# Kernel optimization log

Hardware: AMD Instinct MI355X
Metric: run time of the kernel (lower is better)

## Reference

```python
import jax, jax.numpy as jnp
import numpy as np
from jax import lax


def conv2d(x, w, b=None, pad=1):
    y = lax.conv_general_dilated(x, w, (1, 1), [(pad, pad), (pad, pad)],
                                 dimension_numbers=('NCHW', 'OIHW', 'NCHW'))
    return y if b is None else y + b[None, :, None, None]


def conv3d(x, w, b=None, pad=(0, 0, 0), dil=(1, 1, 1), groups=1):
    y = lax.conv_general_dilated(x, w, (1, 1, 1), [(p, p) for p in pad],
                                 rhs_dilation=dil,
                                 dimension_numbers=('NCDHW', 'OIDHW', 'NCDHW'),
                                 feature_group_count=groups)
    return y if b is None else y + b[None, :, None, None, None]


def base_grid(H, W, dtype):
    # normalized grid, channel 0 = x in [-1,1], channel 1 = y in [-1,1]
    gxn = 2.0 * jnp.arange(W, dtype=dtype) / max(W - 1, 1) - 1.0
    gyn = 2.0 * jnp.arange(H, dtype=dtype) / max(H - 1, 1) - 1.0
    return jnp.stack([jnp.broadcast_to(gxn[None, :], (H, W)),
                      jnp.broadcast_to(gyn[:, None], (H, W))], 0)


def grid_sample(img, grid):
    # img (N,C,H,W), grid (N,H,W,2) in [-1,1] (x,y); bilinear, zeros padding, align_corners=False
    N, C, H, W = img.shape
    gx = ((grid[..., 0] + 1.0) * W - 1.0) * 0.5
    gy = ((grid[..., 1] + 1.0) * H - 1.0) * 0.5
    x0 = jnp.floor(gx)
    y0 = jnp.floor(gy)
    wx = gx - x0
    wy = gy - y0

    def one(im, x0b, y0b, wxb, wyb):
        x0i = x0b.astype(jnp.int32)
        y0i = y0b.astype(jnp.int32)

        def samp(xi, yi):
            valid = (xi >= 0) & (xi < W) & (yi >= 0) & (yi < H)
            v = im[:, jnp.clip(yi, 0, H - 1), jnp.clip(xi, 0, W - 1)]
            return v * valid[None].astype(im.dtype)

        v00 = samp(x0i, y0i)
        v01 = samp(x0i + 1, y0i)
        v10 = samp(x0i, y0i + 1)
        v11 = samp(x0i + 1, y0i + 1)
        return (v00 * (1 - wxb) * (1 - wyb) + v01 * wxb * (1 - wyb)
                + v10 * (1 - wxb) * wyb + v11 * wxb * wyb)

    return jax.vmap(one)(img, x0, y0, wx, wy)


def ms_def_corr(x, y, off):
    # deformable correlation: per scale, warp y by that scale's offset and take
    # the channel-mean dot product with x -> (BT, S, H, W)
    BT, C, H, W = x.shape
    base = base_grid(H, W, x.dtype)
    sc = jnp.array([W - 1, H - 1], x.dtype)[None, :, None, None]
    S = off.shape[1] // 2
    corrs = []
    for i in range(S):
        vg = base[None] + off[:, 2 * i:2 * i + 2] / sc
        w = grid_sample(y, vg.transpose(0, 2, 3, 1))
        corrs.append(jnp.mean(x * w, axis=1))
    return jnp.stack(corrs, 1)


def corr_filter(corr, w1, w2):
    avg = jnp.mean(corr, 1, keepdims=True)
    mx = jnp.max(corr, 1, keepdims=True)
    var = jnp.var(corr, axis=1, keepdims=True, ddof=1)  # torch.var unbiased
    attn = jax.nn.sigmoid(conv2d(jnp.concatenate([avg, mx], 1), w1) + conv2d(var, w2))
    return corr * attn


def setup_inputs() -> dict:
    key = jax.random.key(0)
    ks = jax.random.split(key, 16)
    B, C, T, H, W = 2, 64, 16, 64, 64
    S = 3
    r = C // 16

    def n(k, shape, s=0.02):
        return jax.random.normal(k, shape, jnp.float32) * s

    return {
        'x': jax.random.normal(ks[0], (B, C, T, H, W), jnp.float32),
        'ofs_l_w1': n(ks[1], (C, 2 * C, 3, 3)), 'ofs_l_b1': jnp.zeros((C,), jnp.float32),
        'ofs_l_w2': n(ks[2], (2 * S, C, 3, 3)), 'ofs_l_b2': jnp.zeros((2 * S,), jnp.float32),
        'ofs_r_w1': n(ks[3], (C, 2 * C, 3, 3)), 'ofs_r_b1': jnp.zeros((C,), jnp.float32),
        'ofs_r_w2': n(ks[4], (2 * S, C, 3, 3)), 'ofs_r_b2': jnp.zeros((2 * S,), jnp.float32),
        'cf_w1': n(ks[5], (1, 2, 3, 3), 0.1), 'cf_w2': n(ks[6], (1, 1, 3, 3), 0.1),
        'down_w': n(ks[7], (r, C, 1, 1, 1), 0.1),
        'sa1_w': n(ks[8], (r, 1, 9, 3, 3), 0.1), 'sa1_b': jnp.zeros((r,), jnp.float32),
        'sa2_w': n(ks[9], (r, 1, 9, 3, 3), 0.1), 'sa2_b': jnp.zeros((r,), jnp.float32),
        'sa3_w': n(ks[10], (r, 1, 9, 3, 3), 0.1), 'sa3_b': jnp.zeros((r,), jnp.float32),
        'agg_w': jnp.ones((3,), jnp.float32) / 3,
        'back_w': n(ks[11], (C, r, 1, 1, 1), 0.1),
        'fusion_w': jnp.ones((2,), jnp.float32) / 2,
    }


def reference(x, ofs_l_w1, ofs_l_b1, ofs_l_w2, ofs_l_b2,
              ofs_r_w1, ofs_r_b1, ofs_r_w2, ofs_r_b2,
              cf_w1, cf_w2, down_w,
              sa1_w, sa1_b, sa2_w, sa2_b, sa3_w, sa3_b,
              agg_w, back_w, fusion_w):
    B, C, T, H, W = x.shape
    r = down_w.shape[0]

    # long-term branch: 1x1x1 down conv -> 3 dilated depthwise 3D convs -> 1x1x1 up conv
    x_agg = conv3d(x, down_w)
    agg = (conv3d(x_agg, sa1_w, sa1_b, (4, 1, 1), (1, 1, 1), r) * agg_w[0]
           + conv3d(x_agg, sa2_w, sa2_b, (4, 2, 2), (1, 2, 2), r) * agg_w[1]
           + conv3d(x_agg, sa3_w, sa3_b, (4, 3, 3), (1, 3, 3), r) * agg_w[2])
    long_term = jax.nn.sigmoid(conv3d(agg, back_w)) - 0.5

    # temporal shifts
    left = jnp.concatenate([x[:, :, 1:], x[:, :, -1:]], 2)
    right = jnp.concatenate([x[:, :, :1], x[:, :, :-1]], 2)
    xf = x.transpose(0, 2, 1, 3, 4).reshape(B * T, C, H, W)
    lf = left.transpose(0, 2, 1, 3, 4).reshape(B * T, C, H, W)
    rf = right.transpose(0, 2, 1, 3, 4).reshape(B * T, C, H, W)

    off_lm = conv2d(jax.nn.relu(conv2d(jnp.concatenate([xf, lf], 1), ofs_l_w1, ofs_l_b1)),
                    ofs_l_w2, ofs_l_b2)
    off_rm = conv2d(jax.nn.relu(conv2d(jnp.concatenate([xf, rf], 1), ofs_r_w1, ofs_r_b1)),
                    ofs_r_w2, ofs_r_b2)

    corr_lm = ms_def_corr(xf, lf, off_lm)
    corr_rm = ms_def_corr(xf, rf, off_rm)
    fcl = corr_filter(corr_lm, cf_w1, cf_w2)
    fcr = corr_filter(corr_rm, cf_w1, cf_w2)

    base = base_grid(H, W, x.dtype)
    sc = jnp.array([W - 1, H - 1], x.dtype)[None, :, None, None]
    vg_lm = base[None] + off_lm[:, :2] / sc
    vg_rm = base[None] + off_rm[:, :2] / sc
    warped_lm = grid_sample(lf, vg_lm.transpose(0, 2, 3, 1))
    warped_rm = grid_sample(rf, vg_rm.transpose(0, 2, 3, 1))

    attn_lm = jnp.mean(fcl, 1, keepdims=True)
    attn_rm = jnp.mean(fcr, 1, keepdims=True)
    feat_lm = warped_lm * (jax.nn.sigmoid(attn_lm) - 0.5)
    feat_rm = warped_rm * (jax.nn.sigmoid(attn_rm) - 0.5)

    short = fusion_w[0] * feat_lm + fusion_w[1] * feat_rm
    short = short.reshape(B, T, C, H, W).transpose(0, 2, 1, 3, 4)
    return short * long_term
```

## Files before the change

kernel.cpp:

```cpp
#include <hip/hip_runtime.h>
#include <hip/hip_bf16.h>
#include <math.h>


typedef __attribute__((ext_vector_type(8))) short short8v;
typedef __attribute__((ext_vector_type(4))) float f32x4;

__device__ __forceinline__ float sigmoidf_(float v) {
    return 1.0f / (1.0f + expf(-v));
}

__device__ __forceinline__ float bf2f(short s) {
    union { unsigned u; float f; } z;
    z.u = ((unsigned)(unsigned short)s) << 16;
    return z.f;
}

__device__ __forceinline__ void gll16(const __hip_bfloat16* g, __hip_bfloat16* l) {
    __builtin_amdgcn_global_load_lds((const __attribute__((address_space(1))) unsigned int*)(const void*)g,
                                     (__attribute__((address_space(3))) unsigned int*)(void*)l,
                                     16, 0, 0);
}

struct Samp { int o0, o1, o2, o3; float w0, w1, w2, w3; };

__device__ __forceinline__ Samp make_samp(float ox, float oy, int w, int h) {
    float bx = (2.0f * (float)w) / 63.0f - 1.0f;
    float by = (2.0f * (float)h) / 63.0f - 1.0f;
    float vx = bx + ox / 63.0f;
    float vy = by + oy / 63.0f;
    float gx = ((vx + 1.0f) * 64.0f - 1.0f) * 0.5f;
    float gy = ((vy + 1.0f) * 64.0f - 1.0f) * 0.5f;
    float fx = floorf(gx), fy = floorf(gy);
    float wx = gx - fx, wy = gy - fy;
    int x0 = (int)fx, y0 = (int)fy;
    int x1 = x0 + 1, y1 = y0 + 1;
    bool vx0 = (x0 >= 0) && (x0 < 64), vx1 = (x1 >= 0) && (x1 < 64);
    bool vy0 = (y0 >= 0) && (y0 < 64), vy1 = (y1 >= 0) && (y1 < 64);
    int cx0 = min(max(x0, 0), 63), cx1 = min(max(x1, 0), 63);
    int cy0 = min(max(y0, 0), 63), cy1 = min(max(y1, 0), 63);
    Samp s;
    s.o0 = cy0 * 4224 + (cx0 + 1) * 64; s.w0 = (1.0f - wx) * (1.0f - wy) * ((vx0 && vy0) ? 1.0f : 0.0f);
    s.o1 = cy0 * 4224 + (cx1 + 1) * 64; s.w1 = wx * (1.0f - wy) * ((vx1 && vy0) ? 1.0f : 0.0f);
    s.o2 = cy1 * 4224 + (cx0 + 1) * 64; s.w2 = (1.0f - wx) * wy * ((vx0 && vy1) ? 1.0f : 0.0f);
    s.o3 = cy1 * 4224 + (cx1 + 1) * 64; s.w3 = wx * wy * ((vx1 && vy1) ? 1.0f : 0.0f);
    return s;
}

__global__ __launch_bounds__(256) void k_prep_x(const float* __restrict__ x,
                                                const float* __restrict__ dw,
                                                __hip_bfloat16* __restrict__ xT,
                                                float* __restrict__ xa)
{
    int bid = blockIdx.x;
    int h = bid & 63;
    int n = bid >> 6;
    int b = n >> 4, t = n & 15;
    __shared__ float s[64][65];
    int tid = threadIdx.x;
    for (int idx = tid; idx < 4096; idx += 256) {
        int c = idx >> 6, w = idx & 63;
        s[c][w] = x[(((size_t)b * 64 + c) * 16 + t) * 4096 + h * 64 + w];
    }
    __syncthreads();
    __hip_bfloat16* op = xT + ((size_t)n * 64 + h) * 4224;
    for (int idx = tid; idx < 4224; idx += 256) {
        int wp = idx >> 6, c = idx & 63;
        float v = (wp == 0 || wp == 65) ? 0.f : s[c][wp - 1];
        op[idx] = __float2bfloat16(v);
    }
    int w = tid & 63, g = tid >> 6;
    float acc = 0.f;
    const float* dwg = dw + g * 64;
    #pragma unroll 8
    for (int c = 0; c < 64; c++) acc = fmaf(s[c][w], dwg[c], acc);
    xa[((size_t)(b * 4 + g) * 16 + t) * 4096 + h * 64 + w] = acc;
}

__global__ __launch_bounds__(256) void k_prep_w(const float* __restrict__ wl1,
                                                const float* __restrict__ wr1,
                                                const float* __restrict__ wl2,
                                                const float* __restrict__ wr2,
                                                __hip_bfloat16* __restrict__ Wmisc,
                                                __hip_bfloat16* __restrict__ hidden)
{
    int idx = blockIdx.x * 256 + threadIdx.x;
    if (idx < 147456) {
        int side = (idx >= 73728) ? 1 : 0;
        int i = idx - side * 73728;
        int ci = i & 127;
        int co = (i >> 7) & 63;
        int tap = i >> 13;
        const float* w = side ? wr1 : wl1;
        float v = w[((size_t)co * 128 + ci) * 9 + tap];
        int pos = side * 73728 + tap * 8192 + co * 128 + (ci ^ ((co & 15) << 3));
        Wmisc[pos] = __float2bfloat16(v);
    } else if (idx < 151680) {
        Wmisc[idx] = __float2bfloat16(0.f);
    } else if (idx < 170112) {
        int i2 = idx - 151680;
        int side = i2 / 9216;
        int j = i2 - side * 9216;
        int tap = j >> 10;
        int rem = j & 1023;
        int co = rem >> 6;
        int ci = rem & 63;
        const float* w = side ? wr2 : wl2;
        float v = (co < 6) ? w[((size_t)co * 64 + ci) * 9 + tap] : 0.f;
        Wmisc[idx] = __float2bfloat16(v);
    } else if (idx < 432256) {
        int i3 = idx - 170112;
        int co = i3 & 63;
        int sel = (i3 >> 6) & 1;
        int rr = (i3 >> 7) & 63;
        int nn = i3 >> 13;
        hidden[((size_t)(nn * 64 + rr) * 66 + (sel ? 65 : 0)) * 64 + co] = __float2bfloat16(0.f);
    }
}

__global__ __launch_bounds__(512, 4) void k_conv1_mfma(const __hip_bfloat16* __restrict__ xT,
                                                       const __hip_bfloat16* __restrict__ Wb,
                                                       const __hip_bfloat16* __restrict__ zrow,
                                                       const float* __restrict__ b1,
                                                       __hip_bfloat16* __restrict__ hidden,
                                                       int dir)
{
    __shared__ __hip_bfloat16 sB[24576];

    int bid = blockIdx.x;
    int rq = bid & 15;
    int n = bid >> 4;
    int b = n >> 4, t = n & 15;
    int t2 = (dir > 0) ? min(t + 1, 15) : max(t - 1, 0);
    int n2 = b * 16 + t2;

    int tid = threadIdx.x;
    int wv = tid >> 6;
    int lane = tid & 63;
    int r = rq * 4 + (wv & 3);
    int m0 = (wv >> 2) * 32;
    int lr = lane & 15;
    int q = lane >> 4;
    int lk = q << 3;

    const __hip_bfloat16* fA0 = xT + (size_t)n * 270336;
    const __hip_bfloat16* fA1 = xT + (size_t)n2 * 270336;

    f32x4 acc[2][4];
    #pragma unroll
    for (int ni = 0; ni < 4; ni++) {
        float bb = b1[ni * 16 + lr];
        acc[0][ni] = (f32x4){bb, bb, bb, bb};
        acc[1][ni] = (f32x4){bb, bb, bb, bb};
    }

    int kx[2][2];
    #pragma unroll
    for (int khalf = 0; khalf < 2; khalf++)
        #pragma unroll
        for (int ks = 0; ks < 2; ks++)
            kx[khalf][ks] = ((khalf << 7) + (ks << 6) + (q << 4)) ^ (lr << 4);

    const char* sbc = (const char*)&sB[0];

    #pragma unroll
    for (int g = 0; g < 3; g++) {
        __syncthreads();
        {
            const __hip_bfloat16* wsrc = Wb + (size_t)g * 24576 + wv * 3072 + lane * 8;
            #pragma unroll
            for (int j = 0; j < 6; j++)
                gll16(wsrc + j * 512, &sB[wv * 3072 + j * 512]);
        }
        __syncthreads();

        int rr = r + g - 1;
        bool ok = (rr >= 0) && (rr < 64);
        const __hip_bfloat16* r0 = ok ? (fA0 + rr * 4224) : zrow;
        const __hip_bfloat16* r1 = ok ? (fA1 + rr * 4224) : zrow;

        #pragma unroll
        for (int tl = 0; tl < 3; tl++) {
            int abase = (m0 + lr + tl) * 64 + lk;
            #pragma unroll
            for (int khalf = 0; khalf < 2; khalf++) {
                const __hip_bfloat16* ar = khalf ? r1 : r0;
                short8v a00 = *(const short8v*)(ar + abase);
                short8v a01 = *(const short8v*)(ar + abase + 32);
                short8v a10 = *(const short8v*)(ar + abase + 1024);
                short8v a11 = *(const short8v*)(ar + abase + 1056);
                #pragma unroll
                for (int ni = 0; ni < 4; ni++) {
                    int rowb = tl * 16384 + ni * 4096 + lr * 256;
                    short8v b0  = *(const short8v*)(sbc + (rowb + kx[khalf][0]));
                    short8v b1v = *(const short8v*)(sbc + (rowb + kx[khalf][1]));
                    acc[0][ni] = __builtin_amdgcn_mfma_f32_16x16x32_bf16(a00, b0, acc[0][ni], 0, 0, 0);
                    acc[1][ni] = __builtin_amdgcn_mfma_f32_16x16x32_bf16(a10, b0, acc[1][ni], 0, 0, 0);
                    acc[0][ni] = __builtin_amdgcn_mfma_f32_16x16x32_bf16(a01, b1v, acc[0][ni], 0, 0, 0);
                    acc[1][ni] = __builtin_amdgcn_mfma_f32_16x16x32_bf16(a11, b1v, acc[1][ni], 0, 0, 0);
                }
            }
        }
    }

    int pxq = q << 2;
    __hip_bfloat16* hb = hidden + (size_t)(n * 64 + r) * 66 * 64;
    #pragma unroll
    for (int mi = 0; mi < 2; mi++) {
        #pragma unroll
        for (int ni = 0; ni < 4; ni++) {
            int co = ni * 16 + lr;
            #pragma unroll
            for (int j = 0; j < 4; j++) {
                int px = m0 + mi * 16 + pxq + j;
                float v = acc[mi][ni][j];
                v = v < 0.f ? 0.f : v;
                hb[(size_t)(px + 1) * 64 + co] = __float2bfloat16(v);
            }
        }
    }
}

__global__ __launch_bounds__(256) void k_conv2_mfma(const __hip_bfloat16* __restrict__ hidden,
                                                    const __hip_bfloat16* __restrict__ W2b,
                                                    const __hip_bfloat16* __restrict__ zrow,
                                                    const float* __restrict__ b2,
                                                    float* __restrict__ off)
{
    int bid = blockIdx.x;
    int rq = bid & 15;
    int n = bid >> 4;
    int tid = threadIdx.x;
    int wv = tid >> 6;
    int lane = tid & 63;
    int r = rq * 4 + wv;
    int lr = lane & 15;
    int lk = (lane >> 4) << 3;

    const __hip_bfloat16* hbase = hidden + (size_t)n * 270336;

    float bb = (lr < 6) ? b2[lr] : 0.f;
    f32x4 acc[4];
    #pragma unroll
    for (int mi = 0; mi < 4; mi++) acc[mi] = (f32x4){bb, bb, bb, bb};

    #pragma unroll
    for (int tap = 0; tap < 9; tap++) {
        const int kh = tap / 3, kw = tap - (tap / 3) * 3;
        int rr = r + kh - 1;
        bool ok = (rr >= 0) && (rr < 64);
        const __hip_bfloat16* hr = ok ? (hbase + (size_t)rr * 4224) : zrow;
        const __hip_bfloat16* bw = W2b + ((size_t)tap * 16 + lr) * 64 + lk;
        short8v b0 = *(const short8v*)(bw);
        short8v b1v = *(const short8v*)(bw + 32);
        #pragma unroll
        for (int mi = 0; mi < 4; mi++) {
            int abase = (mi * 16 + lr + kw) * 64 + lk;
            short8v a0 = *(const short8v*)(hr + abase);
            short8v a1 = *(const short8v*)(hr + abase + 32);
            acc[mi] = __builtin_amdgcn_mfma_f32_16x16x32_bf16(a0, b0, acc[mi], 0, 0, 0);
            acc[mi] = __builtin_amdgcn_mfma_f32_16x16x32_bf16(a1, b1v, acc[mi], 0, 0, 0);
        }
    }
    if (lr < 6) {
        int pxq = (lane >> 4) << 2;
        #pragma unroll
        for (int mi = 0; mi < 4; mi++) {
            #pragma unroll
            for (int j = 0; j < 4; j++) {
                int px = mi * 16 + pxq + j;
                off[((size_t)n * 6 + lr) * 4096 + r * 64 + px] = acc[mi][j];
            }
        }
    }
}

__global__ __launch_bounds__(256) void k_agg(const float* __restrict__ xa,
                                             const float* __restrict__ w1, const float* __restrict__ b1,
                                             const float* __restrict__ w2, const float* __restrict__ b2,
                                             const float* __restrict__ w3, const float* __restrict__ b3,
                                             const float* __restrict__ aw,
                                             float* __restrict__ agg)
{
    int gid = blockIdx.x * 256 + threadIdx.x;
    int hw = gid & 4095;
    int rest = gid >> 12;
    int t = rest & 15;
    int g = (rest >> 4) & 3;
    int b = rest >> 6;
    int h = hw >> 6, w = hw & 63;
    const float* base = xa + ((size_t)(b * 4 + g) * 16) * 4096;
    const float* ws0 = w1 + g * 81;
    const float* ws1 = w2 + g * 81;
    const float* ws2 = w3 + g * 81;
    float acc0 = b1[g], acc1 = b2[g], acc2 = b3[g];
    for (int kd = 0; kd < 9; kd++) {
        int d = t + kd - 4;
        if (d < 0 || d > 15) continue;
        const float* fr = base + (size_t)d * 4096;
        #pragma unroll
        for (int kh = 0; kh < 3; kh++) {
            #pragma unroll
            for (int kw = 0; kw < 3; kw++) {
                int widx = kd * 9 + kh * 3 + kw;
                {
                    int yy = h + (kh - 1), xx = w + (kw - 1);
                    if (yy >= 0 && yy < 64 && xx >= 0 && xx < 64)
                        acc0 = fmaf(fr[yy * 64 + xx], ws0[widx], acc0);
                }
                {
                    int yy = h + (kh - 1) * 2, xx = w + (kw - 1) * 2;
                    if (yy >= 0 && yy < 64 && xx >= 0 && xx < 64)
                        acc1 = fmaf(fr[yy * 64 + xx], ws1[widx], acc1);
                }
                {
                    int yy = h + (kh - 1) * 3, xx = w + (kw - 1) * 3;
                    if (yy >= 0 && yy < 64 && xx >= 0 && xx < 64)
                        acc2 = fmaf(fr[yy * 64 + xx], ws2[widx], acc2);
                }
            }
        }
    }
    agg[gid] = acc0 * aw[0] + acc1 * aw[1] + acc2 * aw[2];
}

__global__ __launch_bounds__(256) void k_corr2(const __hip_bfloat16* __restrict__ xT,
                                               const float* __restrict__ off_l,
                                               const float* __restrict__ off_r,
                                               float* __restrict__ stats_l,
                                               float* __restrict__ stats_r)
{
    int tid = threadIdx.x;
    int wv = tid >> 6;
    int lane = tid & 63;
    int pl = lane & 31;
    int ch = lane >> 5;
    int pidx = blockIdx.x * 128 + wv * 32 + pl;
    int half = pidx >> 17;
    int gid = pidx & 131071;
    const float* off = half ? off_r : off_l;
    float* stats = half ? stats_r : stats_l;

    int hw = gid & 4095;
    int n = gid >> 12;
    int b = n >> 4, t = n & 15;
    int t2 = half ? max(t - 1, 0) : min(t + 1, 15);
    int n2 = b * 16 + t2;
    int h = hw >> 6, w = hw & 63;
    int cc0 = ch * 32;

    const __hip_bfloat16* xf = xT + (size_t)n * 270336 + h * 4224 + (w + 1) * 64 + cc0;
    const __hip_bfloat16* yf = xT + (size_t)n2 * 270336 + cc0;

    Samp sp[3];
    #pragma unroll
    for (int s = 0; s < 3; s++) {
        float ox = off[((size_t)n * 6 + 2 * s) * 4096 + hw];
        float oy = off[((size_t)n * 6 + 2 * s + 1) * 4096 + hw];
        sp[s] = make_samp(ox, oy, w, h);
    }

    short8v xv[4];
    #pragma unroll
    for (int i = 0; i < 4; i++) xv[i] = *(const short8v*)(xf + 8 * i);

    float ac[3][4];
    #pragma unroll
    for (int s = 0; s < 3; s++)
        #pragma unroll
        for (int qq = 0; qq < 4; qq++) ac[s][qq] = 0.f;

    #pragma unroll
    for (int s = 0; s < 3; s++) {
        #pragma unroll
        for (int pr = 0; pr < 2; pr++) {
            int oa = pr ? sp[s].o2 : sp[s].o0;
            int ob = pr ? sp[s].o3 : sp[s].o1;
            short8v va[4], vb[4];
            #pragma unroll
            for (int i = 0; i < 4; i++) {
                va[i] = *(const short8v*)(yf + oa + 8 * i);
                vb[i] = *(const short8v*)(yf + ob + 8 * i);
            }
            #pragma unroll
            for (int i = 0; i < 4; i++) {
                #pragma unroll
                for (int e = 0; e < 8; e++) {
                    float xe = bf2f(xv[i][e]);
                    ac[s][pr * 2]     = fmaf(xe, bf2f(va[i][e]), ac[s][pr * 2]);
                    ac[s][pr * 2 + 1] = fmaf(xe, bf2f(vb[i][e]), ac[s][pr * 2 + 1]);
                }
            }
        }
    }

    #pragma unroll
    for (int s = 0; s < 3; s++)
        #pragma unroll
        for (int qq = 0; qq < 4; qq++)
            ac[s][qq] += __shfl_xor(ac[s][qq], 32, 64);

    if (ch == 0) {
        float c[3];
        #pragma unroll
        for (int s = 0; s < 3; s++)
            c[s] = (ac[s][0] * sp[s].w0 + ac[s][1] * sp[s].w1 + ac[s][2] * sp[s].w2 + ac[s][3] * sp[s].w3) * (1.0f / 64.0f);
        float avg = (c[0] + c[1] + c[2]) * (1.0f / 3.0f);
        float mx = fmaxf(c[0], fmaxf(c[1], c[2]));
        float d0 = c[0] - avg, d1 = c[1] - avg, d2 = c[2] - avg;
        float var = (d0 * d0 + d1 * d1 + d2 * d2) * 0.5f;
        stats[(size_t)n * 4096 + hw] = avg;
        stats[131072 + (size_t)n * 4096 + hw] = mx;
        stats[262144 + (size_t)n * 4096 + hw] = var;
    }
}

__device__ __forceinline__ float attn_val(const float* __restrict__ stats, int n, int hw,
                                          const float* __restrict__ cfw1,
                                          const float* __restrict__ cfw2)
{
    int h = hw >> 6, w = hw & 63;
    const float* avg = stats + (size_t)n * 4096;
    const float* mx  = stats + 131072 + (size_t)n * 4096;
    const float* var = stats + 262144 + (size_t)n * 4096;
    float s = 0.f;
    #pragma unroll
    for (int k = 0; k < 9; k++) {
        int kh = k / 3 - 1, kw = k - (k / 3) * 3 - 1;
        int yy = h + kh, xx = w + kw;
        if (yy >= 0 && yy < 64 && xx >= 0 && xx < 64) {
            int p = yy * 64 + xx;
            s += avg[p] * cfw1[k] + mx[p] * cfw1[9 + k] + var[p] * cfw2[k];
        }
    }
    float attn = sigmoidf_(s);
    return sigmoidf_(avg[hw] * attn) - 0.5f;
}

__global__ __launch_bounds__(256) void k_final(const __hip_bfloat16* __restrict__ xT,
                                               const float* __restrict__ off_l,
                                               const float* __restrict__ off_r,
                                               const float* __restrict__ stats_l,
                                               const float* __restrict__ stats_r,
                                               const float* __restrict__ cfw1,
                                               const float* __restrict__ cfw2,
                                               const float* __restrict__ agg,
                                               const float* __restrict__ backw,
                                               const float* __restrict__ fusw,
                                               float* __restrict__ out)
{
    int gid0 = blockIdx.x * 256 + threadIdx.x;
    int hw = gid0 & 4095;
    int ch = (gid0 >> 12) & 1;
    int n = gid0 >> 13;
    int b = n >> 4, t = n & 15;
    int tl = min(t + 1, 15), tr = max(t - 1, 0);
    int nl = b * 16 + tl, nr = b * 16 + tr;
    int h = hw >> 6, w = hw & 63;
    int cc0 = ch * 32;

    float oxl = off_l[((size_t)n * 6 + 0) * 4096 + hw];
    float oyl = off_l[((size_t)n * 6 + 1) * 4096 + hw];
    float oxr = off_r[((size_t)n * 6 + 0) * 4096 + hw];
    float oyr = off_r[((size_t)n * 6 + 1) * 4096 + hw];
    Samp sl = make_samp(oxl, oyl, w, h);
    Samp sr = make_samp(oxr, oyr, w, h);

    const __hip_bfloat16* lf = xT + (size_t)nl * 270336 + cc0;
    const __hip_bfloat16* rf = xT + (size_t)nr * 270336 + cc0;

    short8v lv[4][4], rv[4][4];
    #pragma unroll
    for (int i = 0; i < 4; i++) {
        lv[0][i] = *(const short8v*)(lf + sl.o0 + 8 * i);
        lv[1][i] = *(const short8v*)(lf + sl.o1 + 8 * i);
        lv[2][i] = *(const short8v*)(lf + sl.o2 + 8 * i);
        lv[3][i] = *(const short8v*)(lf + sl.o3 + 8 * i);
        rv[0][i] = *(const short8v*)(rf + sr.o0 + 8 * i);
        rv[1][i] = *(const short8v*)(rf + sr.o1 + 8 * i);
        rv[2][i] = *(const short8v*)(rf + sr.o2 + 8 * i);
        rv[3][i] = *(const short8v*)(rf + sr.o3 + 8 * i);
    }

    float Al = attn_val(stats_l, n, hw, cfw1, cfw2) * fusw[0];
    float Ar = attn_val(stats_r, n, hw, cfw1, cfw2) * fusw[1];

    float ag0 = agg[((size_t)(b * 4 + 0) * 16 + t) * 4096 + hw];
    float ag1 = agg[((size_t)(b * 4 + 1) * 16 + t) * 4096 + hw];
    float ag2 = agg[((size_t)(b * 4 + 2) * 16 + t) * 4096 + hw];
    float ag3 = agg[((size_t)(b * 4 + 3) * 16 + t) * 4096 + hw];

    #pragma unroll
    for (int i = 0; i < 4; i++) {
        #pragma unroll
        for (int e = 0; e < 8; e++) {
            int c = cc0 + i * 8 + e;
            float wl = sl.w0 * bf2f(lv[0][i][e]) + sl.w1 * bf2f(lv[1][i][e])
                     + sl.w2 * bf2f(lv[2][i][e]) + sl.w3 * bf2f(lv[3][i][e]);
            float wr = sr.w0 * bf2f(rv[0][i][e]) + sr.w1 * bf2f(rv[1][i][e])
                     + sr.w2 * bf2f(rv[2][i][e]) + sr.w3 * bf2f(rv[3][i][e]);
            float lt = sigmoidf_(ag0 * backw[c * 4 + 0] + ag1 * backw[c * 4 + 1]
                               + ag2 * backw[c * 4 + 2] + ag3 * backw[c * 4 + 3]) - 0.5f;
            out[(((size_t)b * 64 + c) * 16 + t) * 4096 + hw] = (wl * Al + wr * Ar) * lt;
        }
    }
}

extern "C" void kernel_launch(void* const* d_in, const int* in_sizes, int n_in,
                              void* d_out, int out_size, void* d_ws, size_t ws_size,
                              hipStream_t stream)
{
    const float* x     = (const float*)d_in[0];
    const float* lw1   = (const float*)d_in[1];
    const float* lb1   = (const float*)d_in[2];
    const float* lw2   = (const float*)d_in[3];
    const float* lb2   = (const float*)d_in[4];
    const float* rw1   = (const float*)d_in[5];
    const float* rb1   = (const float*)d_in[6];
    const float* rw2   = (const float*)d_in[7];
    const float* rb2   = (const float*)d_in[8];
    const float* cfw1  = (const float*)d_in[9];
    const float* cfw2  = (const float*)d_in[10];
    const float* downw = (const float*)d_in[11];
    const float* sa1w  = (const float*)d_in[12];
    const float* sa1b  = (const float*)d_in[13];
    const float* sa2w  = (const float*)d_in[14];
    const float* sa2b  = (const float*)d_in[15];
    const float* sa3w  = (const float*)d_in[16];
    const float* sa3b  = (const float*)d_in[17];
    const float* aggw  = (const float*)d_in[18];
    const float* backw = (const float*)d_in[19];
    const float* fusw  = (const float*)d_in[20];
    float* out = (float*)d_out;

    float* ws      = (float*)d_ws;
    float* x_agg   = ws;
    float* agg     = x_agg + 524288;
    float* off_l   = agg + 524288;
    float* off_r   = off_l + 786432;
    float* stats_l = off_r + 786432;
    float* stats_r = stats_l + 393216;
    __hip_bfloat16* hidden = (__hip_bfloat16*)(stats_r + 393216);
    __hip_bfloat16* xT     = hidden + 8650752;
    __hip_bfloat16* Wmisc  = xT + 8650752;
    __hip_bfloat16* Wb     = Wmisc;
    __hip_bfloat16* zrow   = Wmisc + 147456;
    __hip_bfloat16* W2bL   = Wmisc + 151680;
    __hip_bfloat16* W2bR   = W2bL + 9216;

    k_prep_x<<<2048, 256, 0, stream>>>(x, downw, xT, x_agg);
    k_prep_w<<<1689, 256, 0, stream>>>(lw1, rw1, lw2, rw2, Wmisc, hidden);

    k_agg<<<2048, 256, 0, stream>>>(x_agg, sa1w, sa1b, sa2w, sa2b, sa3w, sa3b, aggw, agg);

    k_conv1_mfma<<<512, 512, 0, stream>>>(xT, Wb, zrow, lb1, hidden, +1);
    k_conv2_mfma<<<512, 256, 0, stream>>>(hidden, W2bL, zrow, lb2, off_l);

    k_conv1_mfma<<<512, 512, 0, stream>>>(xT, Wb + 73728, zrow, rb1, hidden, -1);
    k_conv2_mfma<<<512, 256, 0, stream>>>(hidden, W2bR, zrow, rb2, off_r);

    k_corr2<<<2048, 256, 0, stream>>>(xT, off_l, off_r, stats_l, stats_r);

    k_final<<<1024, 256, 0, stream>>>(xT, off_l, off_r, stats_l, stats_r, cfw1, cfw2,
                                      agg, backw, fusw, out);
}
```

Measured before the change: 258.5 us.

## Merge left/right conv launches into one grid and re-split corr2 channel work

Left and right offset branches of conv1 and conv2 now run in a single launch of twice the blocks, with a separate hidden buffer per side when the workspace is large enough. Otherwise they fall back to sequential launches. Zeroing of the hidden padding columns moves from the weight-prep kernel into conv1. The correlation kernel now gives each pixel four 16-channel lanes instead of two 32-channel lanes, doubling the grid and interleaving loads across scales to expose more memory parallelism. This trades a larger workspace and extra shuffles for fewer launches and more occupancy.

```diff
diff --git a/kernel.cpp b/kernel.cpp
--- a/kernel.cpp
+++ b/kernel.cpp
@@ -5,6 +5,8 @@
 
 typedef __attribute__((ext_vector_type(8))) short short8v;
 typedef __attribute__((ext_vector_type(4))) float f32x4;
+
+#define HID_ELEMS 8650752ULL
 
 __device__ __forceinline__ float sigmoidf_(float v) {
     return 1.0f / (1.0f + expf(-v));
@@ -81,8 +83,7 @@
                                                 const float* __restrict__ wr1,
                                                 const float* __restrict__ wl2,
                                                 const float* __restrict__ wr2,
-                                                __hip_bfloat16* __restrict__ Wmisc,
-                                                __hip_bfloat16* __restrict__ hidden)
+                                                __hip_bfloat16* __restrict__ Wmisc)
 {
     int idx = blockIdx.x * 256 + threadIdx.x;
     if (idx < 147456) {
@@ -108,31 +109,31 @@
         const float* w = side ? wr2 : wl2;
         float v = (co < 6) ? w[((size_t)co * 64 + ci) * 9 + tap] : 0.f;
         Wmisc[idx] = __float2bfloat16(v);
-    } else if (idx < 432256) {
-        int i3 = idx - 170112;
-        int co = i3 & 63;
-        int sel = (i3 >> 6) & 1;
-        int rr = (i3 >> 7) & 63;
-        int nn = i3 >> 13;
-        hidden[((size_t)(nn * 64 + rr) * 66 + (sel ? 65 : 0)) * 64 + co] = __float2bfloat16(0.f);
     }
 }
 
 __global__ __launch_bounds__(512, 4) void k_conv1_mfma(const __hip_bfloat16* __restrict__ xT,
                                                        const __hip_bfloat16* __restrict__ Wb,
                                                        const __hip_bfloat16* __restrict__ zrow,
-                                                       const float* __restrict__ b1,
+                                                       const float* __restrict__ b1l,
+                                                       const float* __restrict__ b1r,
                                                        __hip_bfloat16* __restrict__ hidden,
-                                                       int dir)
+                                                       int side_base, size_t hid_stride)
 {
     __shared__ __hip_bfloat16 sB[24576];
 
     int bid = blockIdx.x;
-    int rq = bid & 15;
-    int n = bid >> 4;
+    int side = side_base + (bid >> 9);
+    int bid2 = bid & 511;
+    int rq = bid2 & 15;
+    int n = bid2 >> 4;
     int b = n >> 4, t = n & 15;
-    int t2 = (dir > 0) ? min(t + 1, 15) : max(t - 1, 0);
+    int t2 = side ? max(t - 1, 0) : min(t + 1, 15);
     int n2 = b * 16 + t2;
+
+    const __hip_bfloat16* WbS = Wb + (size_t)side * 73728;
+    const float* b1 = side ? b1r : b1l;
+    __hip_bfloat16* hs = hidden + (size_t)side * hid_stride;
 
     int tid = threadIdx.x;
     int wv = tid >> 6;
@@ -167,7 +168,7 @@
     for (int g = 0; g < 3; g++) {
         __syncthreads();
         {
-            const __hip_bfloat16* wsrc = Wb + (size_t)g * 24576 + wv * 3072 + lane * 8;
+            const __hip_bfloat16* wsrc = WbS + (size_t)g * 24576 + wv * 3072 + lane * 8;
             #pragma unroll
             for (int j = 0; j < 6; j++)
                 gll16(wsrc + j * 512, &sB[wv * 3072 + j * 512]);
@@ -204,7 +205,7 @@
     }
 
     int pxq = q << 2;
-    __hip_bfloat16* hb = hidden + (size_t)(n * 64 + r) * 66 * 64;
+    __hip_bfloat16* hb = hs + (size_t)(n * 64 + r) * 4224;
     #pragma unroll
     for (int mi = 0; mi < 2; mi++) {
         #pragma unroll
@@ -219,17 +220,27 @@
             }
         }
     }
+    {
+        int row_l = tid >> 7;
+        int sel = (tid >> 6) & 1;
+        int co = tid & 63;
+        hs[(size_t)(n * 64 + rq * 4 + row_l) * 4224 + (sel ? 65 : 0) * 64 + co] = __float2bfloat16(0.f);
+    }
 }
 
 __global__ __launch_bounds__(256) void k_conv2_mfma(const __hip_bfloat16* __restrict__ hidden,
                                                     const __hip_bfloat16* __restrict__ W2b,
                                                     const __hip_bfloat16* __restrict__ zrow,
-                                                    const float* __restrict__ b2,
-                                                    float* __restrict__ off)
+                                                    const float* __restrict__ b2l,
+                                                    const float* __restrict__ b2r,
+                                                    float* __restrict__ off,
+                                                    int side_base, size_t hid_stride)
 {
     int bid = blockIdx.x;
-    int rq = bid & 15;
-    int n = bid >> 4;
+    int side = side_base + (bid >> 9);
+    int bid2 = bid & 511;
+    int rq = bid2 & 15;
+    int n = bid2 >> 4;
     int tid = threadIdx.x;
     int wv = tid >> 6;
     int lane = tid & 63;
@@ -237,7 +248,10 @@
     int lr = lane & 15;
     int lk = (lane >> 4) << 3;
 
-    const __hip_bfloat16* hbase = hidden + (size_t)n * 270336;
+    const __hip_bfloat16* W2bS = W2b + (size_t)side * 9216;
+    const float* b2 = side ? b2r : b2l;
+    float* offS = off + (size_t)side * 786432;
+    const __hip_bfloat16* hbase = hidden + (size_t)side * hid_stride + (size_t)n * 270336;
 
     float bb = (lr < 6) ? b2[lr] : 0.f;
     f32x4 acc[4];
@@ -250,7 +264,7 @@
         int rr = r + kh - 1;
         bool ok = (rr >= 0) && (rr < 64);
         const __hip_bfloat16* hr = ok ? (hbase + (size_t)rr * 4224) : zrow;
-        const __hip_bfloat16* bw = W2b + ((size_t)tap * 16 + lr) * 64 + lk;
+        const __hip_bfloat16* bw = W2bS + ((size_t)tap * 16 + lr) * 64 + lk;
         short8v b0 = *(const short8v*)(bw);
         short8v b1v = *(const short8v*)(bw + 32);
         #pragma unroll
@@ -269,7 +283,7 @@
             #pragma unroll
             for (int j = 0; j < 4; j++) {
                 int px = mi * 16 + pxq + j;
-                off[((size_t)n * 6 + lr) * 4096 + r * 64 + px] = acc[mi][j];
+                offS[((size_t)n * 6 + lr) * 4096 + r * 64 + px] = acc[mi][j];
             }
         }
     }
@@ -324,18 +338,18 @@
     agg[gid] = acc0 * aw[0] + acc1 * aw[1] + acc2 * aw[2];
 }
 
-__global__ __launch_bounds__(256) void k_corr2(const __hip_bfloat16* __restrict__ xT,
-                                               const float* __restrict__ off_l,
-                                               const float* __restrict__ off_r,
-                                               float* __restrict__ stats_l,
-                                               float* __restrict__ stats_r)
+__global__ __launch_bounds__(256, 4) void k_corr2(const __hip_bfloat16* __restrict__ xT,
+                                                  const float* __restrict__ off_l,
+                                                  const float* __restrict__ off_r,
+                                                  float* __restrict__ stats_l,
+                                                  float* __restrict__ stats_r)
 {
     int tid = threadIdx.x;
     int wv = tid >> 6;
     int lane = tid & 63;
-    int pl = lane & 31;
-    int ch = lane >> 5;
-    int pidx = blockIdx.x * 128 + wv * 32 + pl;
+    int pl = lane & 15;
+    int cq = lane >> 4;
+    int pidx = blockIdx.x * 64 + wv * 16 + pl;
     int half = pidx >> 17;
     int gid = pidx & 131071;
     const float* off = half ? off_r : off_l;
@@ -347,7 +361,7 @@
     int t2 = half ? max(t - 1, 0) : min(t + 1, 15);
     int n2 = b * 16 + t2;
     int h = hw >> 6, w = hw & 63;
-    int cc0 = ch * 32;
+    int cc0 = cq * 16;
 
     const __hip_bfloat16* xf = xT + (size_t)n * 270336 + h * 4224 + (w + 1) * 64 + cc0;
     const __hip_bfloat16* yf = xT + (size_t)n2 * 270336 + cc0;
@@ -360,51 +374,77 @@
         sp[s] = make_samp(ox, oy, w, h);
     }
 
-    short8v xv[4];
-    #pragma unroll
-    for (int i = 0; i < 4; i++) xv[i] = *(const short8v*)(xf + 8 * i);
+    short8v xv0 = *(const short8v*)(xf);
+    short8v xv1 = *(const short8v*)(xf + 8);
+
+    int o0[4] = {sp[0].o0, sp[0].o1, sp[0].o2, sp[0].o3};
+    int o1[4] = {sp[1].o0, sp[1].o1, sp[1].o2, sp[1].o3};
+    int o2[4] = {sp[2].o0, sp[2].o1, sp[2].o2, sp[2].o3};
+
+    short8v y0[4][2], y1[4][2], y2[4][2];
+    #pragma unroll
+    for (int cr = 0; cr < 4; cr++) {
+        y0[cr][0] = *(const short8v*)(yf + o0[cr]);
+        y0[cr][1] = *(const short8v*)(yf + o0[cr] + 8);
+    }
+    #pragma unroll
+    for (int cr = 0; cr < 4; cr++) {
+        y1[cr][0] = *(const short8v*)(yf + o1[cr]);
+        y1[cr][1] = *(const short8v*)(yf + o1[cr] + 8);
+    }
+
+    float xs[16];
+    #pragma unroll
+    for (int e = 0; e < 8; e++) { xs[e] = bf2f(xv0[e]); xs[8 + e] = bf2f(xv1[e]); }
 
     float ac[3][4];
     #pragma unroll
     for (int s = 0; s < 3; s++)
         #pragma unroll
-        for (int qq = 0; qq < 4; qq++) ac[s][qq] = 0.f;
-
-    #pragma unroll
-    for (int s = 0; s < 3; s++) {
-        #pragma unroll
-        for (int pr = 0; pr < 2; pr++) {
-            int oa = pr ? sp[s].o2 : sp[s].o0;
-            int ob = pr ? sp[s].o3 : sp[s].o1;
-            short8v va[4], vb[4];
-            #pragma unroll
-            for (int i = 0; i < 4; i++) {
-                va[i] = *(const short8v*)(yf + oa + 8 * i);
-                vb[i] = *(const short8v*)(yf + ob + 8 * i);
-            }
-            #pragma unroll
-            for (int i = 0; i < 4; i++) {
-                #pragma unroll
-                for (int e = 0; e < 8; e++) {
-                    float xe = bf2f(xv[i][e]);
-                    ac[s][pr * 2]     = fmaf(xe, bf2f(va[i][e]), ac[s][pr * 2]);
-                    ac[s][pr * 2 + 1] = fmaf(xe, bf2f(vb[i][e]), ac[s][pr * 2 + 1]);
-                }
-            }
-        }
-    }
+        for (int cr = 0; cr < 4; cr++) ac[s][cr] = 0.f;
+
+    #pragma unroll
+    for (int cr = 0; cr < 4; cr++)
+        #pragma unroll
+        for (int i = 0; i < 2; i++)
+            #pragma unroll
+            for (int e = 0; e < 8; e++)
+                ac[0][cr] = fmaf(xs[i * 8 + e], bf2f(y0[cr][i][e]), ac[0][cr]);
+    #pragma unroll
+    for (int cr = 0; cr < 4; cr++) {
+        y2[cr][0] = *(const short8v*)(yf + o2[cr]);
+        y2[cr][1] = *(const short8v*)(yf + o2[cr] + 8);
+    }
+    #pragma unroll
+    for (int cr = 0; cr < 4; cr++)
+        #pragma unroll
+        for (int i = 0; i < 2; i++)
+            #pragma unroll
+            for (int e = 0; e < 8; e++)
+                ac[1][cr] = fmaf(xs[i * 8 + e], bf2f(y1[cr][i][e]), ac[1][cr]);
+    #pragma unroll
+    for (int cr = 0; cr < 4; cr++)
+        #pragma unroll
+        for (int i = 0; i < 2; i++)
+            #pragma unroll
+            for (int e = 0; e < 8; e++)
+                ac[2][cr] = fmaf(xs[i * 8 + e], bf2f(y2[cr][i][e]), ac[2][cr]);
 
     #pragma unroll
     for (int s = 0; s < 3; s++)
         #pragma unroll
-        for (int qq = 0; qq < 4; qq++)
-            ac[s][qq] += __shfl_xor(ac[s][qq], 32, 64);
-
-    if (ch == 0) {
+        for (int cr = 0; cr < 4; cr++) {
+            float v = ac[s][cr];
+            v += __shfl_xor(v, 16, 64);
+            v += __shfl_xor(v, 32, 64);
+            ac[s][cr] = v;
+        }
+
+    if (cq == 0) {
         float c[3];
-        #pragma unroll
-        for (int s = 0; s < 3; s++)
-            c[s] = (ac[s][0] * sp[s].w0 + ac[s][1] * sp[s].w1 + ac[s][2] * sp[s].w2 + ac[s][3] * sp[s].w3) * (1.0f / 64.0f);
+        c[0] = (ac[0][0] * sp[0].w0 + ac[0][1] * sp[0].w1 + ac[0][2] * sp[0].w2 + ac[0][3] * sp[0].w3) * (1.0f / 64.0f);
+        c[1] = (ac[1][0] * sp[1].w0 + ac[1][1] * sp[1].w1 + ac[1][2] * sp[1].w2 + ac[1][3] * sp[1].w3) * (1.0f / 64.0f);
+        c[2] = (ac[2][0] * sp[2].w0 + ac[2][1] * sp[2].w1 + ac[2][2] * sp[2].w2 + ac[2][3] * sp[2].w3) * (1.0f / 64.0f);
         float avg = (c[0] + c[1] + c[2]) * (1.0f / 3.0f);
         float mx = fmaxf(c[0], fmaxf(c[1], c[2]));
         float d0 = c[0] - avg, d1 = c[1] - avg, d2 = c[2] - avg;
@@ -540,26 +580,34 @@
     float* off_r   = off_l + 786432;
     float* stats_l = off_r + 786432;
     float* stats_r = stats_l + 393216;
-    __hip_bfloat16* hidden = (__hip_bfloat16*)(stats_r + 393216);
-    __hip_bfloat16* xT     = hidden + 8650752;
-    __hip_bfloat16* Wmisc  = xT + 8650752;
-    __hip_bfloat16* Wb     = Wmisc;
-    __hip_bfloat16* zrow   = Wmisc + 147456;
-    __hip_bfloat16* W2bL   = Wmisc + 151680;
-    __hip_bfloat16* W2bR   = W2bL + 9216;
+    __hip_bfloat16* hidden  = (__hip_bfloat16*)(stats_r + 393216);
+    __hip_bfloat16* xT      = hidden + HID_ELEMS;
+    __hip_bfloat16* Wmisc   = xT + HID_ELEMS;
+    __hip_bfloat16* Wb      = Wmisc;
+    __hip_bfloat16* zrow    = Wmisc + 147456;
+    __hip_bfloat16* W2bL    = Wmisc + 151680;
+    __hip_bfloat16* hidden2 = Wmisc + 170112;
+
+    const size_t need_merged = 65876224ULL;
+    const bool merged = (ws_size >= need_merged);
+    const size_t hid_stride = merged ? (size_t)(hidden2 - hidden) : 0;
 
     k_prep_x<<<2048, 256, 0, stream>>>(x, downw, xT, x_agg);
-    k_prep_w<<<1689, 256, 0, stream>>>(lw1, rw1, lw2, rw2, Wmisc, hidden);
+    k_prep_w<<<665, 256, 0, stream>>>(lw1, rw1, lw2, rw2, Wmisc);
 
     k_agg<<<2048, 256, 0, stream>>>(x_agg, sa1w, sa1b, sa2w, sa2b, sa3w, sa3b, aggw, agg);
 
-    k_conv1_mfma<<<512, 512, 0, stream>>>(xT, Wb, zrow, lb1, hidden, +1);
-    k_conv2_mfma<<<512, 256, 0, stream>>>(hidden, W2bL, zrow, lb2, off_l);
-
-    k_conv1_mfma<<<512, 512, 0, stream>>>(xT, Wb + 73728, zrow, rb1, hidden, -1);
-    k_conv2_mfma<<<512, 256, 0, stream>>>(hidden, W2bR, zrow, rb2, off_r);
-
-    k_corr2<<<2048, 256, 0, stream>>>(xT, off_l, off_r, stats_l, stats_r);
+    if (merged) {
+        k_conv1_mfma<<<1024, 512, 0, stream>>>(xT, Wb, zrow, lb1, rb1, hidden, 0, hid_stride);
+        k_conv2_mfma<<<1024, 256, 0, stream>>>(hidden, W2bL, zrow, lb2, rb2, off_l, 0, hid_stride);
+    } else {
+        k_conv1_mfma<<<512, 512, 0, stream>>>(xT, Wb, zrow, lb1, rb1, hidden, 0, 0);
+        k_conv2_mfma<<<512, 256, 0, stream>>>(hidden, W2bL, zrow, lb2, rb2, off_l, 0, 0);
+        k_conv1_mfma<<<512, 512, 0, stream>>>(xT, Wb, zrow, lb1, rb1, hidden, 1, 0);
+        k_conv2_mfma<<<512, 256, 0, stream>>>(hidden, W2bL, zrow, lb2, rb2, off_l, 1, 0);
+    }
+
+    k_corr2<<<4096, 256, 0, stream>>>(xT, off_l, off_r, stats_l, stats_r);
 
     k_final<<<1024, 256, 0, stream>>>(xT, off_l, off_r, stats_l, stats_r, cfw1, cfw2,
                                       agg, backw, fusw, out);
```

Result: no change. 259.3 us (+0.3%).
